# Kernel tuning notes

Hardware: AMD Instinct MI355X
Metric: run time of the kernel (lower is better)

The kernel has to match this reference:

```python
import jax, jax.numpy as jnp
import numpy as np

THRESHOLD = 1e-3  # hardcoded `thresholds = 0.001` in the sparse branch


def setup_inputs() -> dict:
    key = jax.random.key(0)
    k1, k2, k3, k4, k5 = jax.random.split(key, 5)
    b, r, d_in, d_out = 8, 4096, 768, 768
    x = jax.random.normal(k1, (b, r, d_in), dtype=jnp.float32)
    weight = jax.random.normal(k2, (d_out, d_in), dtype=jnp.float32) * 0.02
    bias = jax.random.normal(k3, (d_out,), dtype=jnp.float32) * 0.02
    U = jax.random.normal(k4, (d_in, d_in), dtype=jnp.float32) * (d_in ** -0.5)
    VT = jax.random.normal(k5, (d_out, d_out), dtype=jnp.float32) * (d_out ** -0.5)
    return {"x": x, "weight": weight, "bias": bias, "U": U, "VT": VT}


def reference(x, weight, bias, U, VT):
    # Sparse path (len_grads >= 30) of LinearFunctionSparseGrad.forward.
    # h = x @ U.T, rotated into the gradient basis.  [b, r, c]
    h = jnp.einsum('brc,dc->brd', x, U)
    # Threshold-sparsify: zero entries with |h| <= 0.001.
    h = jnp.where(jnp.abs(h) > THRESHOLD, h, jnp.zeros((), h.dtype))
    # Original: gather nonzero rows/cols, h[rows][:, cols] @ weight.T[cols],
    # then scatter back via I[:, rows] @ res_. Dropped cols are exactly-zero
    # columns and dropped rows are exactly-zero rows, so the math equals a
    # dense matmul on the masked tensor (no [b*r, b*r] identity needed).
    res = jnp.einsum('brc,oc->bro', h, weight)        # h @ weight.T
    res = jnp.einsum('bro,po->brp', res, VT)          # res_ @ VT.T (self.VT=VT_orig.T => VT here)
    return res + bias
```

## Files before the change

kernel.cpp:

```cpp
#include <hip/hip_runtime.h>
#include <hip/hip_bf16.h>

typedef __bf16 bf16_t;
typedef bf16_t bf16x8 __attribute__((ext_vector_type(8)));
typedef bf16_t bf16x4 __attribute__((ext_vector_type(4)));
typedef float  f32x4  __attribute__((ext_vector_type(4)));

#define BM 128
#define BN 128
#define BK 64

enum { EPI_NONE = 0, EPI_THRESH = 1, EPI_BIAS = 2 };


template <int EPI, typename CT>
__device__ __forceinline__
void gemm_tile(const bf16_t* __restrict__ A, const bf16_t* __restrict__ B,
               CT* __restrict__ C, const float* __restrict__ bias,
               int m0, int n0, int N, int K,
               bf16_t* As, bf16_t* Bs)
{
    const int lane = threadIdx.x & 63;
    const int wave = threadIdx.x >> 6;
    const int wm = wave >> 1;
    const int wn = wave & 1;

    const int srow = lane >> 3;
    const int scg  = (lane & 7) ^ ((lane >> 3) & 7);

    const int fm = lane & 15;
    const int q  = lane >> 4;
    const int fsw = fm & 7;

    f32x4 acc[4][4];
#pragma unroll
    for (int i = 0; i < 4; i++)
#pragma unroll
        for (int j = 0; j < 4; j++) acc[i][j] = {0.f, 0.f, 0.f, 0.f};

    for (int k0 = 0; k0 < K; k0 += BK) {
#pragma unroll
        for (int i = 0; i < 4; i++) {
            const int ubase = wave * 256 + i * 64;
            const int row   = (ubase >> 3) + srow;
            const bf16_t* ga = A + (size_t)(m0 + row) * K + k0 + scg * 8;
            __builtin_amdgcn_global_load_lds(
                (const __attribute__((address_space(1))) void*)ga,
                (__attribute__((address_space(3))) void*)(As + (size_t)ubase * 8),
                16, 0, 0);
            const bf16_t* gb = B + (size_t)(n0 + row) * K + k0 + scg * 8;
            __builtin_amdgcn_global_load_lds(
                (const __attribute__((address_space(1))) void*)gb,
                (__attribute__((address_space(3))) void*)(Bs + (size_t)ubase * 8),
                16, 0, 0);
        }
        __syncthreads();

#pragma unroll
        for (int h = 0; h < 2; h++) {
            bf16x8 af[4], bfr[4];
#pragma unroll
            for (int i = 0; i < 4; i++) {
                const int row = wm * 64 + i * 16 + fm;
                af[i] = *(const bf16x8*)(As + (size_t)(row * 8 + ((h * 4 + q) ^ fsw)) * 8);
            }
#pragma unroll
            for (int j = 0; j < 4; j++) {
                const int row = wn * 64 + j * 16 + fm;
                bfr[j] = *(const bf16x8*)(Bs + (size_t)(row * 8 + ((h * 4 + q) ^ fsw)) * 8);
            }
#pragma unroll
            for (int i = 0; i < 4; i++)
#pragma unroll
                for (int j = 0; j < 4; j++)
                    acc[i][j] = __builtin_amdgcn_mfma_f32_16x16x32_bf16(
                        af[i], bfr[j], acc[i][j], 0, 0, 0);
        }
        __syncthreads();
    }

#pragma unroll
    for (int i = 0; i < 4; i++) {
#pragma unroll
        for (int j = 0; j < 4; j++) {
            const int col = n0 + wn * 64 + j * 16 + fm;
            float bv = 0.f;
            if (EPI == EPI_BIAS) bv = bias[col];
#pragma unroll
            for (int r = 0; r < 4; r++) {
                const int row = m0 + wm * 64 + i * 16 + q * 4 + r;
                float v = acc[i][j][r];
                if (EPI == EPI_THRESH) v = (fabsf(v) > 1e-3f) ? v : 0.f;
                if (EPI == EPI_BIAS) v += bv;
                C[(size_t)row * N + col] = (CT)v;
            }
        }
    }
}

__global__ __launch_bounds__(256)
void gemm_h_wc(const bf16_t* __restrict__ xb, const bf16_t* __restrict__ Ub,
               bf16_t* __restrict__ h,
               const bf16_t* __restrict__ VTb, const bf16_t* __restrict__ Wt,
               bf16_t* __restrict__ Wc)
{
    __shared__ __align__(16) bf16_t As[BM * BK];
    __shared__ __align__(16) bf16_t Bs[BN * BK];
    const int b = blockIdx.x;
    if (b < 1536) {
        gemm_tile<EPI_THRESH, bf16_t>(xb, Ub, h, nullptr,
                                      (b / 6) * BM, (b % 6) * BN, 768, 768, As, Bs);
    } else {
        const int b2 = b - 1536;
        gemm_tile<EPI_NONE, bf16_t>(VTb, Wt, Wc, nullptr,
                                    (b2 / 6) * BM, (b2 % 6) * BN, 768, 768, As, Bs);
    }
}

__global__ __launch_bounds__(256)
void gemm_out(const bf16_t* __restrict__ h, const bf16_t* __restrict__ Wc,
              float* __restrict__ out, const float* __restrict__ bias)
{
    __shared__ __align__(16) bf16_t As[BM * BK];
    __shared__ __align__(16) bf16_t Bs[BN * BK];
    const int b = blockIdx.x;
    gemm_tile<EPI_BIAS, float>(h, Wc, out, bias,
                               (b / 6) * BM, (b % 6) * BN, 768, 768, As, Bs);
}

__global__ __launch_bounds__(256)
void prep(const float* __restrict__ x, const float* __restrict__ U,
          const float* __restrict__ VT, const float* __restrict__ w,
          bf16_t* __restrict__ xb, bf16_t* __restrict__ Ub,
          bf16_t* __restrict__ VTb, bf16_t* __restrict__ Wt)
{
    __shared__ float tt[32][33];
    const int b = blockIdx.x;
    if (b < 25728) {
        const float* src; bf16_t* dst; int i;
        if (b < 24576)      { src = x;  dst = xb;  i = b * 256 + threadIdx.x; }
        else if (b < 25152) { src = U;  dst = Ub;  i = (b - 24576) * 256 + threadIdx.x; }
        else                { src = VT; dst = VTb; i = (b - 25152) * 256 + threadIdx.x; }
        const f32x4 v = ((const f32x4*)src)[i];
        bf16x4 o;
        o[0] = (bf16_t)v[0]; o[1] = (bf16_t)v[1];
        o[2] = (bf16_t)v[2]; o[3] = (bf16_t)v[3];
        ((bf16x4*)dst)[i] = o;
    } else {
        const int t = b - 25728;
        const int bx = (t % 24) * 32, by = (t / 24) * 32;
        const int tx = threadIdx.x & 31, ty = threadIdx.x >> 5;
#pragma unroll
        for (int i = 0; i < 32; i += 8)
            tt[ty + i][tx] = w[(size_t)(by + ty + i) * 768 + bx + tx];
        __syncthreads();
#pragma unroll
        for (int i = 0; i < 32; i += 8)
            Wt[(size_t)(bx + ty + i) * 768 + by + tx] = (bf16_t)tt[tx][ty + i];
    }
}

extern "C" void kernel_launch(void* const* d_in, const int* in_sizes, int n_in,
                              void* d_out, int out_size, void* d_ws, size_t ws_size,
                              hipStream_t stream)
{
    const float* x    = (const float*)d_in[0];
    const float* w    = (const float*)d_in[1];
    const float* bias = (const float*)d_in[2];
    const float* U    = (const float*)d_in[3];
    const float* VT   = (const float*)d_in[4];
    float* out = (float*)d_out;

    const int D = 768;
    const int M = 8 * 4096;
    const size_t MD = (size_t)M * D;
    const size_t DD = (size_t)D * D;

    char* ws = (char*)d_ws;
    bf16_t* xb  = (bf16_t*)ws;
    bf16_t* h   = (bf16_t*)(ws + MD * 2);
    bf16_t* Ub  = (bf16_t*)(ws + MD * 4);
    bf16_t* VTb = (bf16_t*)(ws + MD * 4 + DD * 2);
    bf16_t* Wt  = (bf16_t*)(ws + MD * 4 + DD * 4);
    bf16_t* Wc  = (bf16_t*)(ws + MD * 4 + DD * 6);

    prep<<<26304, 256, 0, stream>>>(x, U, VT, w, xb, Ub, VTb, Wt);
    gemm_h_wc<<<1536 + 36, 256, 0, stream>>>(xb, Ub, h, VTb, Wt, Wc);
    gemm_out<<<1536, 256, 0, stream>>>(h, Wc, out, bias);
}
```

Baseline: 313.0 us.

## Fuse prep and GEMMs into one persistent cooperative kernel with grid syncs

```diff
diff --git a/kernel.cpp b/kernel.cpp
--- a/kernel.cpp
+++ b/kernel.cpp
@@ -1,89 +1,94 @@
 #include <hip/hip_runtime.h>
+#include <hip/hip_cooperative_groups.h>
 #include <hip/hip_bf16.h>
+
+namespace cg = cooperative_groups;
 
 typedef __bf16 bf16_t;
 typedef bf16_t bf16x8 __attribute__((ext_vector_type(8)));
-typedef bf16_t bf16x4 __attribute__((ext_vector_type(4)));
 typedef float  f32x4  __attribute__((ext_vector_type(4)));
 
 #define BM 128
-#define BN 128
-#define BK 64
+#define BN 96
+#define BK 32
 
 enum { EPI_NONE = 0, EPI_THRESH = 1, EPI_BIAS = 2 };
-
 
 template <int EPI, typename CT>
 __device__ __forceinline__
 void gemm_tile(const bf16_t* __restrict__ A, const bf16_t* __restrict__ B,
                CT* __restrict__ C, const float* __restrict__ bias,
-               int m0, int n0, int N, int K,
-               bf16_t* As, bf16_t* Bs)
+               int m0, int n0, bf16_t* As, bf16_t* Bs)
 {
     const int lane = threadIdx.x & 63;
     const int wave = threadIdx.x >> 6;
     const int wm = wave >> 1;
     const int wn = wave & 1;
 
-    const int srow = lane >> 3;
-    const int scg  = (lane & 7) ^ ((lane >> 3) & 7);
+    const int srow = lane >> 2;
+    const int scol = (lane & 3) ^ (srow & 3);
 
     const int fm = lane & 15;
     const int q  = lane >> 4;
-    const int fsw = fm & 7;
-
-    f32x4 acc[4][4];
+    const int fsw = q ^ (fm & 3);
+
+    f32x4 acc[4][3];
 #pragma unroll
     for (int i = 0; i < 4; i++)
 #pragma unroll
-        for (int j = 0; j < 4; j++) acc[i][j] = {0.f, 0.f, 0.f, 0.f};
-
-    for (int k0 = 0; k0 < K; k0 += BK) {
+        for (int j = 0; j < 3; j++) acc[i][j] = {0.f, 0.f, 0.f, 0.f};
+
+    for (int k0 = 0; k0 < 768; k0 += BK) {
+#pragma unroll
+        for (int i = 0; i < 2; i++) {
+            const int u   = wave * 128 + i * 64;
+            const int row = (u >> 2) + srow;
+            const bf16_t* g = A + (size_t)(m0 + row) * 768 + k0 + scol * 8;
+            __builtin_amdgcn_global_load_lds(
+                (const __attribute__((address_space(1))) void*)g,
+                (__attribute__((address_space(3))) void*)(As + (size_t)u * 8),
+                16, 0, 0);
+        }
+#pragma unroll
+        for (int i = 0; i < 2; i++) {
+            const int jj = wave + i * 4;
+            if (jj < 6) {
+                const int u   = jj * 64;
+                const int row = jj * 16 + srow;
+                const bf16_t* g = B + (size_t)(n0 + row) * 768 + k0 + scol * 8;
+                __builtin_amdgcn_global_load_lds(
+                    (const __attribute__((address_space(1))) void*)g,
+                    (__attribute__((address_space(3))) void*)(Bs + (size_t)u * 8),
+                    16, 0, 0);
+            }
+        }
+        __syncthreads();
+
+        bf16x8 af[4], bfr[3];
 #pragma unroll
         for (int i = 0; i < 4; i++) {
-            const int ubase = wave * 256 + i * 64;
-            const int row   = (ubase >> 3) + srow;
-            const bf16_t* ga = A + (size_t)(m0 + row) * K + k0 + scg * 8;
-            __builtin_amdgcn_global_load_lds(
-                (const __attribute__((address_space(1))) void*)ga,
-                (__attribute__((address_space(3))) void*)(As + (size_t)ubase * 8),
-                16, 0, 0);
-            const bf16_t* gb = B + (size_t)(n0 + row) * K + k0 + scg * 8;
-            __builtin_amdgcn_global_load_lds(
-                (const __attribute__((address_space(1))) void*)gb,
-                (__attribute__((address_space(3))) void*)(Bs + (size_t)ubase * 8),
-                16, 0, 0);
-        }
-        __syncthreads();
-
-#pragma unroll
-        for (int h = 0; h < 2; h++) {
-            bf16x8 af[4], bfr[4];
-#pragma unroll
-            for (int i = 0; i < 4; i++) {
-                const int row = wm * 64 + i * 16 + fm;
-                af[i] = *(const bf16x8*)(As + (size_t)(row * 8 + ((h * 4 + q) ^ fsw)) * 8);
-            }
-#pragma unroll
-            for (int j = 0; j < 4; j++) {
-                const int row = wn * 64 + j * 16 + fm;
-                bfr[j] = *(const bf16x8*)(Bs + (size_t)(row * 8 + ((h * 4 + q) ^ fsw)) * 8);
-            }
-#pragma unroll
-            for (int i = 0; i < 4; i++)
-#pragma unroll
-                for (int j = 0; j < 4; j++)
-                    acc[i][j] = __builtin_amdgcn_mfma_f32_16x16x32_bf16(
-                        af[i], bfr[j], acc[i][j], 0, 0, 0);
-        }
+            const int r = wm * 64 + i * 16 + fm;
+            af[i] = *(const bf16x8*)(As + (size_t)(r * 4 + fsw) * 8);
+        }
+#pragma unroll
+        for (int j = 0; j < 3; j++) {
+            const int r = wn * 48 + j * 16 + fm;
+            bfr[j] = *(const bf16x8*)(Bs + (size_t)(r * 4 + fsw) * 8);
+        }
+#pragma unroll
+        for (int i = 0; i < 4; i++)
+#pragma unroll
+            for (int j = 0; j < 3; j++)
+                acc[i][j] = __builtin_amdgcn_mfma_f32_16x16x32_bf16(
+                    af[i], bfr[j], acc[i][j], 0, 0, 0);
         __syncthreads();
     }
 
 #pragma unroll
     for (int i = 0; i < 4; i++) {
 #pragma unroll
-        for (int j = 0; j < 4; j++) {
-            const int col = n0 + wn * 64 + j * 16 + fm;
+        for (int j = 0; j < 3; j++) {
+            const int col = n0 + wn * 48 + j * 16 + fm;
             float bv = 0.f;
             if (EPI == EPI_BIAS) bv = bias[col];
 #pragma unroll
@@ -92,64 +97,49 @@
                 float v = acc[i][j][r];
                 if (EPI == EPI_THRESH) v = (fabsf(v) > 1e-3f) ? v : 0.f;
                 if (EPI == EPI_BIAS) v += bv;
-                C[(size_t)row * N + col] = (CT)v;
+                C[(size_t)row * 768 + col] = (CT)v;
             }
         }
     }
 }
 
-__global__ __launch_bounds__(256)
-void gemm_h_wc(const bf16_t* __restrict__ xb, const bf16_t* __restrict__ Ub,
-               bf16_t* __restrict__ h,
-               const bf16_t* __restrict__ VTb, const bf16_t* __restrict__ Wt,
-               bf16_t* __restrict__ Wc)
-{
+__device__ __forceinline__
+void cvt8(const float* __restrict__ src, bf16_t* __restrict__ dst, long i)
+{
+    const f32x4 a = ((const f32x4*)src)[2 * i];
+    const f32x4 b = ((const f32x4*)src)[2 * i + 1];
+    bf16x8 o;
+    o[0] = (bf16_t)a[0]; o[1] = (bf16_t)a[1]; o[2] = (bf16_t)a[2]; o[3] = (bf16_t)a[3];
+    o[4] = (bf16_t)b[0]; o[5] = (bf16_t)b[1]; o[6] = (bf16_t)b[2]; o[7] = (bf16_t)b[3];
+    ((bf16x8*)dst)[i] = o;
+}
+
+__global__ __launch_bounds__(256, 4)
+void fused(const float* __restrict__ x, const float* __restrict__ w,
+           const float* __restrict__ bias, const float* __restrict__ U,
+           const float* __restrict__ VT,
+           bf16_t* __restrict__ xb, bf16_t* __restrict__ h,
+           bf16_t* __restrict__ Ub, bf16_t* __restrict__ VTb,
+           bf16_t* __restrict__ Wt, bf16_t* __restrict__ Wc,
+           float* __restrict__ out)
+{
+    cg::grid_group grid = cg::this_grid();
     __shared__ __align__(16) bf16_t As[BM * BK];
     __shared__ __align__(16) bf16_t Bs[BN * BK];
-    const int b = blockIdx.x;
-    if (b < 1536) {
-        gemm_tile<EPI_THRESH, bf16_t>(xb, Ub, h, nullptr,
-                                      (b / 6) * BM, (b % 6) * BN, 768, 768, As, Bs);
-    } else {
-        const int b2 = b - 1536;
-        gemm_tile<EPI_NONE, bf16_t>(VTb, Wt, Wc, nullptr,
-                                    (b2 / 6) * BM, (b2 % 6) * BN, 768, 768, As, Bs);
-    }
-}
-
-__global__ __launch_bounds__(256)
-void gemm_out(const bf16_t* __restrict__ h, const bf16_t* __restrict__ Wc,
-              float* __restrict__ out, const float* __restrict__ bias)
-{
-    __shared__ __align__(16) bf16_t As[BM * BK];
-    __shared__ __align__(16) bf16_t Bs[BN * BK];
-    const int b = blockIdx.x;
-    gemm_tile<EPI_BIAS, float>(h, Wc, out, bias,
-                               (b / 6) * BM, (b % 6) * BN, 768, 768, As, Bs);
-}
-
-__global__ __launch_bounds__(256)
-void prep(const float* __restrict__ x, const float* __restrict__ U,
-          const float* __restrict__ VT, const float* __restrict__ w,
-          bf16_t* __restrict__ xb, bf16_t* __restrict__ Ub,
-          bf16_t* __restrict__ VTb, bf16_t* __restrict__ Wt)
-{
     __shared__ float tt[32][33];
-    const int b = blockIdx.x;
-    if (b < 25728) {
-        const float* src; bf16_t* dst; int i;
-        if (b < 24576)      { src = x;  dst = xb;  i = b * 256 + threadIdx.x; }
-        else if (b < 25152) { src = U;  dst = Ub;  i = (b - 24576) * 256 + threadIdx.x; }
-        else                { src = VT; dst = VTb; i = (b - 25152) * 256 + threadIdx.x; }
-        const f32x4 v = ((const f32x4*)src)[i];
-        bf16x4 o;
-        o[0] = (bf16_t)v[0]; o[1] = (bf16_t)v[1];
-        o[2] = (bf16_t)v[2]; o[3] = (bf16_t)v[3];
-        ((bf16x4*)dst)[i] = o;
-    } else {
-        const int t = b - 25728;
+
+    const int G = gridDim.x;
+    const int gtid = blockIdx.x * 256 + threadIdx.x;
+    const int gstr = G * 256;
+
+    for (int i = gtid; i < 2 * 73728; i += gstr) {
+        if (i < 73728) cvt8(U, Ub, i);
+        else           cvt8(VT, VTb, i - 73728);
+    }
+    for (int t = blockIdx.x; t < 576; t += G) {
         const int bx = (t % 24) * 32, by = (t / 24) * 32;
         const int tx = threadIdx.x & 31, ty = threadIdx.x >> 5;
+        __syncthreads();
 #pragma unroll
         for (int i = 0; i < 32; i += 8)
             tt[ty + i][tx] = w[(size_t)(by + ty + i) * 768 + bx + tx];
@@ -158,6 +148,28 @@
         for (int i = 0; i < 32; i += 8)
             Wt[(size_t)(bx + ty + i) * 768 + by + tx] = (bf16_t)tt[tx][ty + i];
     }
+    grid.sync();
+
+    if (blockIdx.x < 48) {
+        const int t = blockIdx.x;
+        gemm_tile<EPI_NONE, bf16_t>(VTb, Wt, Wc, nullptr,
+                                    (t >> 3) * BM, (t & 7) * BN, As, Bs);
+    } else {
+        const long t2 = (long)(blockIdx.x - 48) * 256 + threadIdx.x;
+        const long s2 = (long)(G - 48) * 256;
+        for (long i = t2; i < 3145728; i += s2)
+            cvt8(x, xb, i);
+    }
+    grid.sync();
+
+    for (int t = blockIdx.x; t < 2048; t += G)
+        gemm_tile<EPI_THRESH, bf16_t>(xb, Ub, h, nullptr,
+                                      (t >> 3) * BM, (t & 7) * BN, As, Bs);
+    grid.sync();
+
+    for (int t = blockIdx.x; t < 2048; t += G)
+        gemm_tile<EPI_BIAS, float>(h, Wc, out, bias,
+                                   (t >> 3) * BM, (t & 7) * BN, As, Bs);
 }
 
 extern "C" void kernel_launch(void* const* d_in, const int* in_sizes, int n_in,
@@ -184,7 +196,14 @@
     bf16_t* Wt  = (bf16_t*)(ws + MD * 4 + DD * 4);
     bf16_t* Wc  = (bf16_t*)(ws + MD * 4 + DD * 6);
 
-    prep<<<26304, 256, 0, stream>>>(x, U, VT, w, xb, Ub, VTb, Wt);
-    gemm_h_wc<<<1536 + 36, 256, 0, stream>>>(xb, Ub, h, VTb, Wt, Wc);
-    gemm_out<<<1536, 256, 0, stream>>>(h, Wc, out, bias);
-}
+    int nb = 0;
+    hipOccupancyMaxActiveBlocksPerMultiprocessor(&nb, fused, 256, 0);
+    if (nb < 1) nb = 1;
+    int G = 256 * nb;
+    if (G > 1024) G = 1024;
+
+    void* args[] = {(void*)&x, (void*)&w, (void*)&bias, (void*)&U, (void*)&VT,
+                    (void*)&xb, (void*)&h, (void*)&Ub, (void*)&VTb,
+                    (void*)&Wt, (void*)&Wc, (void*)&out};
+    hipLaunchCooperativeKernel(fused, dim3(G), dim3(256), args, 0, stream);
+}
```

Result: slower. 551.4 us (+76.1%).
